# Performance work log

Measured on AMD Instinct MI355X. Metric: run time of the kernel, lower is better.

Reference implementation:

```python
import jax, jax.numpy as jnp
import numpy as np
import math

DIM, SCALES, ORIENTS, K = 32, 3, 8, 15
SIGMA, GAMMA = 5.0, 0.5
B, H, W = 4, 128, 128

def _make_gabor_filters():
    # matches EnhancedBlockGabor._create_complex_filters
    coords = np.arange(-(K // 2), K // 2 + 1, dtype=np.float32)
    y, x = np.meshgrid(coords, coords, indexing='ij')  # torch.meshgrid default 'ij'
    filts = []
    for s in range(SCALES):
        fu = 1.0 / 2 ** s
        for o in range(ORIENTS):
            theta = o * math.pi / ORIENTS
            xt = x * math.cos(theta) + y * math.sin(theta)
            yt = -x * math.sin(theta) + y * math.cos(theta)
            env = np.exp(-(xt ** 2 + GAMMA ** 2 * yt ** 2) / (2 * SIGMA ** 2))
            amp = fu ** 2 / (math.pi * GAMMA ** 2)
            real = amp * env * np.cos(2 * math.pi * fu * xt)
            imag = amp * env * np.sin(2 * math.pi * fu * xt)
            filts.append(np.stack([real, imag]))
    return jnp.asarray(np.stack(filts), dtype=jnp.float32)  # (S*O, 2, K, K)

def setup_inputs() -> dict:
    key = jax.random.key(0)
    k1, k2, k3 = jax.random.split(key, 3)
    x = jax.random.normal(k1, (B, DIM, H, W), dtype=jnp.float32)
    filters = _make_gabor_filters()
    cin = DIM * SCALES * ORIENTS
    w1 = jax.random.normal(k2, (DIM, cin), dtype=jnp.float32) / np.sqrt(cin)
    b1 = jax.random.normal(k3, (DIM,), dtype=jnp.float32) * 0.01
    return {"x": x, "filters": filters, "w1": w1, "b1": b1}

def reference(x, filters, w1, b1):
    Bb, C, Hh, Ww = x.shape
    SO = filters.shape[0]
    pad = K // 2
    # depthwise multi-scale Gabor conv: every channel vs every (scale,orient,re/im) filter
    xr = x.reshape(Bb * C, 1, Hh, Ww)
    kern = filters.reshape(SO * 2, 1, K, K)
    feat = jax.lax.conv_general_dilated(
        xr, kern, window_strides=(1, 1), padding=[(pad, pad), (pad, pad)],
        dimension_numbers=('NCHW', 'OIHW', 'NCHW'))  # (B*C, SO*2, H, W)
    feat = feat.reshape(Bb, C, SO, 2, Hh, Ww)
    mag = jnp.sqrt(feat[:, :, :, 0] ** 2 + feat[:, :, :, 1] ** 2)  # (B,C,SO,H,W)
    mag = jnp.swapaxes(mag, -1, -2)  # original permutes H<->W before reshape
    mag = mag.reshape(Bb, C * SO, Hh, Ww)
    y = jnp.einsum('oc,bchw->bohw', w1, mag) + b1[None, :, None, None]
    mean = y.mean(axis=(2, 3), keepdims=True)
    var = y.var(axis=(2, 3), keepdims=True)
    return (y - mean) / jnp.sqrt(var + 1e-5)  # InstanceNorm2d (affine=False)
```

## Files before the change

### kernel.cpp

```cpp
#include <hip/hip_runtime.h>


typedef __attribute__((ext_vector_type(8))) short bfx8;
typedef __attribute__((ext_vector_type(4))) float fx4;
typedef __attribute__((ext_vector_type(4))) unsigned ux4;

#define NREP   2
#define RPITCH 144
#define RROWS  144
#define IMG_SH (RROWS * RPITCH)
#define REP_SH (128 * IMG_SH)
#define XREP_SH (NREP * REP_SH)

#define A_OFF    ((size_t)XREP_SH * 2)
#define W1B_OFF  (A_OFF + (size_t)48 * 256 * 2)
#define YP_OFF   (W1B_OFF + (size_t)32 * 32 * 32 * 2)
#define ST_OFF   (YP_OFF + (size_t)128 * 16384 * 4)

#define WROW_DW  40
#define WREP_DW  656
#define WBUF_DW  (2 * WREP_DW)
#define WWAVE_DW (2 * WBUF_DW)

__device__ __forceinline__ unsigned short f2bf(float f) {
    unsigned u = __float_as_uint(f);
    u = (u + 0x7FFFu + ((u >> 16) & 1u)) >> 16;
    return (unsigned short)u;
}

__device__ __forceinline__ float fsqrt(float x) {
    float r;
    asm("v_sqrt_f32 %0, %1" : "=v"(r) : "v"(x));
    return r;
}

__global__ void prep(const float* __restrict__ x, const float* __restrict__ filt,
                     const float* __restrict__ w1, unsigned* __restrict__ xrep,
                     unsigned short* __restrict__ A, unsigned short* __restrict__ w1b,
                     float* __restrict__ stats)
{
    const int bid = blockIdx.x;
    if (bid < 2048) {
        const int phi = bid & 1, img = (bid >> 1) & 127, rg = bid >> 8;
        const unsigned obase = (unsigned)phi * (REP_SH / 2) + img * (IMG_SH / 2)
                             + rg * 18 * 72;
        for (int j = threadIdx.x; j < 18 * 72; j += 256) {
            int jr = j / 72;
            int pd = j - jr * 72;
            int r  = rg * 18 + jr;
            int c0 = 2 * pd + phi;
            float v0 = 0.f, v1 = 0.f;
            int rr = r - 7;
            if (rr >= 0 && rr < 128) {
                const float* row = x + ((size_t)img * 128 + rr) * 128;
                int cc0 = c0 - 7;
                if (cc0 >= 0 && cc0 < 128) v0 = row[cc0];
                int cc1 = c0 - 6;
                if (cc1 >= 0 && cc1 < 128) v1 = row[cc1];
            }
            xrep[obase + j] = (unsigned)f2bf(v0) | ((unsigned)f2bf(v1) << 16);
        }
    } else {
        int t = (bid - 2048) * 256 + threadIdx.x;
        if (t < 48 * 256) {
            int f = t >> 8, k = t & 255;
            int ky = k >> 4, kx = k & 15;
            float v = 0.f;
            if (ky < 15 && kx < 15) v = filt[(f * 15 + ky) * 15 + kx];
            A[t] = f2bf(v);
        } else if (t < 48 * 256 + 32 * 32 * 32) {
            int j = t - 48 * 256;
            int c = j >> 10, o = (j >> 5) & 31, so = j & 31;
            float v = (so < 24) ? w1[o * 768 + c * 24 + so] : 0.f;
            w1b[j] = f2bf(v);
        } else if (t < 48 * 256 + 32 * 32 * 32 + 256) {
            stats[t - (48 * 256 + 32 * 32 * 32)] = 0.f;
        }
    }
}

__global__ void __attribute__((amdgpu_waves_per_eu(2, 2)))
__launch_bounds__(256)
conv_mix(const unsigned short* __restrict__ xrep,
         const unsigned short* __restrict__ Aw,
         const unsigned short* __restrict__ w1b,
         float* __restrict__ ypart, float* __restrict__ stats)
{
    __shared__ unsigned stagew[4 * WWAVE_DW];
    __shared__ unsigned mag_lds[4][32][20];
    __shared__ float stat_lds[4][4][16];

    const int tid  = threadIdx.x;
    const int lane = tid & 63;
    const int wave = tid >> 6;
    const int n    = lane & 15;
    const int q    = lane >> 4;

    const int bid = blockIdx.x;
    const int b   = (bid >> 1) & 3;
    const int h   = (bid & 1) * 64 + (bid >> 3);

    if (lane < 32) {
        ux4 z4 = {0u, 0u, 0u, 0u};
        *(ux4*)&mag_lds[wave][lane][12] = z4;
    }

    ux4 afr[3][8];
#pragma unroll
    for (int mt = 0; mt < 3; ++mt)
#pragma unroll
        for (int s = 0; s < 8; ++s)
            afr[mt][s] = *(const ux4*)(Aw + ((mt * 16 + n) * 256 + s * 32 + q * 8));
#pragma unroll
    for (int mt = 0; mt < 3; ++mt)
#pragma unroll
        for (int s = 0; s < 8; ++s)
            asm volatile("" : "+v"(afr[mt][s]));

    const int px0 = wave * 32;
    const int p   = n & 1;
    const int fbase = wave * WWAVE_DW + p * WREP_DW + (q >> 1) * WROW_DW
                    + ((n - p) >> 1) + (q & 1) * 4;

    int g_off[3], l_off[3];
#pragma unroll
    for (int i = 0; i < 3; ++i) {
        int slot = i * 64 + lane;
        int rep  = slot >= 96;
        int rem  = slot - 96 * rep;
        int row  = rem / 6;
        int sl   = rem - row * 6;
        g_off[i] = rep * REP_SH + (h + row) * RPITCH + px0 + sl * 8;
        l_off[i] = wave * WWAVE_DW + rep * WREP_DW + row * WROW_DW + sl * 4;
    }
    const int imgbase0 = (b * 32) * IMG_SH;

    const fx4 zero4 = {0.f, 0.f, 0.f, 0.f};
    fx4 yacc[2][2];
#pragma unroll
    for (int mt = 0; mt < 2; ++mt)
#pragma unroll
        for (int t = 0; t < 2; ++t) yacc[mt][t] = zero4;

    {
        const unsigned short* g = xrep + imgbase0;
#pragma unroll
        for (int i = 0; i < 3; ++i)
            *(ux4*)&stagew[l_off[i]] = *(const ux4*)(g + g_off[i]);
    }

    for (int c = 0; c < 32; ++c) {
        ux4 nv[3];
        if (c < 31) {
            const unsigned short* g = xrep + imgbase0 + (c + 1) * IMG_SH;
#pragma unroll
            for (int i = 0; i < 3; ++i)
                nv[i] = *(const ux4*)(g + g_off[i]);
        }

        bfx8 wf[2];
#pragma unroll
        for (int mt = 0; mt < 2; ++mt)
            wf[mt] = *(const bfx8*)(w1b + ((c * 32 + mt * 16 + n) * 32 + q * 8));

        const int fb = fbase + (c & 1) * WBUF_DW;
        ux4 braw[2][8];
#pragma unroll
        for (int s = 0; s < 8; ++s)
#pragma unroll
            for (int t = 0; t < 2; ++t) {
                const int ix = fb + s * (2 * WROW_DW) + t * 8;
                ux4 v = {stagew[ix], stagew[ix + 1], stagew[ix + 2], stagew[ix + 3]};
                braw[t][s] = v;
            }
#pragma unroll
        for (int s = 0; s < 8; ++s)
#pragma unroll
            for (int t = 0; t < 2; ++t)
                asm volatile("" : "+v"(braw[t][s]));

        fx4 cacc[3][2];
#pragma unroll
        for (int mt = 0; mt < 3; ++mt)
#pragma unroll
            for (int t = 0; t < 2; ++t) cacc[mt][t] = zero4;

#pragma unroll
        for (int s = 0; s < 8; ++s)
#pragma unroll
            for (int t = 0; t < 2; ++t) {
                bfx8 bf = __builtin_bit_cast(bfx8, braw[t][s]);
#pragma unroll
                for (int mt = 0; mt < 3; ++mt)
                    cacc[mt][t] = __builtin_amdgcn_mfma_f32_16x16x32_bf16(
                        __builtin_bit_cast(bfx8, afr[mt][s]), bf, cacc[mt][t], 0, 0, 0);
            }

#pragma unroll
        for (int t = 0; t < 2; ++t)
#pragma unroll
            for (int mt = 0; mt < 3; ++mt) {
                float m0 = fsqrt(cacc[mt][t][0] * cacc[mt][t][0] +
                                 cacc[mt][t][1] * cacc[mt][t][1]);
                float m1 = fsqrt(cacc[mt][t][2] * cacc[mt][t][2] +
                                 cacc[mt][t][3] * cacc[mt][t][3]);
                unsigned u0 = __float_as_uint(m0), u1 = __float_as_uint(m1);
                unsigned pk = ((u0 + 0x8000u) >> 16) | ((u1 + 0x8000u) & 0xFFFF0000u);
                mag_lds[wave][t * 16 + n][4 * mt + q] = pk;
            }

#pragma unroll
        for (int t = 0; t < 2; ++t) {
            ux4 raw = *(const ux4*)&mag_lds[wave][t * 16 + n][q * 4];
            bfx8 mb = __builtin_bit_cast(bfx8, raw);
#pragma unroll
            for (int mt = 0; mt < 2; ++mt)
                yacc[mt][t] = __builtin_amdgcn_mfma_f32_16x16x32_bf16(
                    wf[mt], mb, yacc[mt][t], 0, 0, 0);
        }

        if (c < 31) {
            const int wb = ((c + 1) & 1) * WBUF_DW;
#pragma unroll
            for (int i = 0; i < 3; ++i)
                *(ux4*)&stagew[wb + l_off[i]] = nv[i];
        }
    }

    float* yp = ypart + (size_t)(b * 32) * 16384 + h * 128;
#pragma unroll
    for (int mt = 0; mt < 2; ++mt)
#pragma unroll
        for (int t = 0; t < 2; ++t) {
            const int w0 = px0 + t * 16 + n;
#pragma unroll
            for (int r = 0; r < 4; ++r)
                yp[(size_t)(mt * 16 + 4 * q + r) * 16384 + w0] = yacc[mt][t][r];
        }

    float sv[8], qv[8];
#pragma unroll
    for (int mt = 0; mt < 2; ++mt)
#pragma unroll
        for (int r = 0; r < 4; ++r) {
            float v0 = yacc[mt][0][r], v1 = yacc[mt][1][r];
            sv[mt * 4 + r] = v0 + v1;
            qv[mt * 4 + r] = v0 * v0 + v1 * v1;
        }
#pragma unroll
    for (int m = 1; m <= 8; m <<= 1)
#pragma unroll
        for (int i = 0; i < 8; ++i) {
            sv[i] += __shfl_xor(sv[i], m);
            qv[i] += __shfl_xor(qv[i], m);
        }
    if (n == 0) {
#pragma unroll
        for (int i = 0; i < 8; ++i) {
            stat_lds[wave][q][i]     = sv[i];
            stat_lds[wave][q][i + 8] = qv[i];
        }
    }
    __syncthreads();
    if (tid < 64) {
        int qq = tid >> 4, i = tid & 15;
        float acc = stat_lds[0][qq][i] + stat_lds[1][qq][i] +
                    stat_lds[2][qq][i] + stat_lds[3][qq][i];
        int kind = i >> 3, mt = (i >> 2) & 1, r = i & 3;
        int o = mt * 16 + 4 * qq + r;
        atomicAdd(&stats[(b * 32 + o) * 2 + kind], acc);
    }
}

__global__ void inorm2(const float* __restrict__ ypart, const float* __restrict__ stats,
                       float* __restrict__ out)
{
    const int bid = blockIdx.x;
    const int bo = bid >> 4, tile = bid & 15;
    const int h0 = (tile >> 2) * 32, w0 = (tile & 3) * 32;
    const float mean = stats[bo * 2] * (1.f / 16384.f);
    float var = stats[bo * 2 + 1] * (1.f / 16384.f) - mean * mean;
    const float rstd = rsqrtf(fmaxf(var, 0.f) + 1e-5f);

    const float* y0 = ypart + (size_t)bo * 16384;
    __shared__ float tilebuf[32][33];
    const int r = threadIdx.x >> 3, c4 = (threadIdx.x & 7) * 4;

    const size_t base = (size_t)(h0 + r) * 128 + w0 + c4;
    fx4 a = *(const fx4*)(y0 + base);
#pragma unroll
    for (int j = 0; j < 4; ++j)
        tilebuf[r][c4 + j] = (a[j] - mean) * rstd;
    __syncthreads();
    float* ob = out + (size_t)bo * 16384 + (size_t)(w0 + r) * 128 + h0 + c4;
    fx4 o4;
#pragma unroll
    for (int j = 0; j < 4; ++j) o4[j] = tilebuf[c4 + j][r];
    *(fx4*)ob = o4;
}

extern "C" void kernel_launch(void* const* d_in, const int* in_sizes, int n_in,
                              void* d_out, int out_size, void* d_ws, size_t ws_size,
                              hipStream_t stream)
{
    const float* x    = (const float*)d_in[0];
    const float* filt = (const float*)d_in[1];
    const float* w1   = (const float*)d_in[2];
    float* out = (float*)d_out;
    char* ws = (char*)d_ws;

    unsigned*       xrep  = (unsigned*)ws;
    unsigned short* Aw    = (unsigned short*)(ws + A_OFF);
    unsigned short* w1b   = (unsigned short*)(ws + W1B_OFF);
    float*          yp    = (float*)(ws + YP_OFF);
    float*          stats = (float*)(ws + ST_OFF);

    prep<<<2048 + 178, 256, 0, stream>>>(x, filt, w1, xrep, Aw, w1b, stats);
    conv_mix<<<512, 256, 0, stream>>>((const unsigned short*)xrep, Aw, w1b, yp, stats);
    inorm2<<<2048, 256, 0, stream>>>(yp, stats, out);
}
```

Baseline: 127.2 us.

## Software-pipeline mixing MFMA one channel behind and stream B-fragment LDS loads

Double-buffers the per-wave magnitude LDS tile so that the 1x1 mixing MFMAs for channel c-1 run inside the Gabor conv MFMA loop of channel c. This hides the LDS write-then-read dependency. The B-fragment loads become a two-deep rolling prefetch per k-step instead of loading all 8 steps up front, which lowers VGPR pressure. The cost is extra LDS for the second magnitude buffer, a carried weight register pair, and an epilogue for the last channel. Less upfront loading could expose LDS latency if the scheduler does not overlap it.

Measured after the change: 126.2 us. Within noise of the previous version (-0.8%).

```diff
diff --git a/kernel.cpp b/kernel.cpp
--- a/kernel.cpp
+++ b/kernel.cpp
@@ -87,7 +87,7 @@
          float* __restrict__ ypart, float* __restrict__ stats)
 {
     __shared__ unsigned stagew[4 * WWAVE_DW];
-    __shared__ unsigned mag_lds[4][32][20];
+    __shared__ unsigned mag_lds[2][4][32][20];
     __shared__ float stat_lds[4][4][16];
 
     const int tid  = threadIdx.x;
@@ -102,7 +102,8 @@
 
     if (lane < 32) {
         ux4 z4 = {0u, 0u, 0u, 0u};
-        *(ux4*)&mag_lds[wave][lane][12] = z4;
+        *(ux4*)&mag_lds[0][wave][lane][12] = z4;
+        *(ux4*)&mag_lds[1][wave][lane][12] = z4;
     }
 
     ux4 afr[3][8];
@@ -149,6 +150,8 @@
             *(ux4*)&stagew[l_off[i]] = *(const ux4*)(g + g_off[i]);
     }
 
+    bfx8 wfp[2];
+
     for (int c = 0; c < 32; ++c) {
         ux4 nv[3];
         if (c < 31) {
@@ -158,43 +161,64 @@
                 nv[i] = *(const ux4*)(g + g_off[i]);
         }
 
-        bfx8 wf[2];
+        ux4 magp[2];
+        if (c > 0) {
+            const int pbuf = (c & 1) ^ 1;
+#pragma unroll
+            for (int t = 0; t < 2; ++t)
+                magp[t] = *(const ux4*)&mag_lds[pbuf][wave][t * 16 + n][q * 4];
+        }
+
+        bfx8 wfc[2];
 #pragma unroll
         for (int mt = 0; mt < 2; ++mt)
-            wf[mt] = *(const bfx8*)(w1b + ((c * 32 + mt * 16 + n) * 32 + q * 8));
+            wfc[mt] = *(const bfx8*)(w1b + ((c * 32 + mt * 16 + n) * 32 + q * 8));
 
         const int fb = fbase + (c & 1) * WBUF_DW;
-        ux4 braw[2][8];
-#pragma unroll
-        for (int s = 0; s < 8; ++s)
+        ux4 braw[2][2];
+#pragma unroll
+        for (int t = 0; t < 2; ++t) {
+            const int ix = fb + t * 8;
+            ux4 v = {stagew[ix], stagew[ix + 1], stagew[ix + 2], stagew[ix + 3]};
+            braw[0][t] = v;
+        }
+
+        fx4 cacc[3][2];
+#pragma unroll
+        for (int mt = 0; mt < 3; ++mt)
+#pragma unroll
+            for (int t = 0; t < 2; ++t) cacc[mt][t] = zero4;
+
+#pragma unroll
+        for (int s = 0; s < 8; ++s) {
+            if (s < 7) {
+#pragma unroll
+                for (int t = 0; t < 2; ++t) {
+                    const int ix = fb + (s + 1) * (2 * WROW_DW) + t * 8;
+                    ux4 v = {stagew[ix], stagew[ix + 1],
+                             stagew[ix + 2], stagew[ix + 3]};
+                    braw[(s + 1) & 1][t] = v;
+                }
+            }
 #pragma unroll
             for (int t = 0; t < 2; ++t) {
-                const int ix = fb + s * (2 * WROW_DW) + t * 8;
-                ux4 v = {stagew[ix], stagew[ix + 1], stagew[ix + 2], stagew[ix + 3]};
-                braw[t][s] = v;
-            }
-#pragma unroll
-        for (int s = 0; s < 8; ++s)
-#pragma unroll
-            for (int t = 0; t < 2; ++t)
-                asm volatile("" : "+v"(braw[t][s]));
-
-        fx4 cacc[3][2];
-#pragma unroll
-        for (int mt = 0; mt < 3; ++mt)
-#pragma unroll
-            for (int t = 0; t < 2; ++t) cacc[mt][t] = zero4;
-
-#pragma unroll
-        for (int s = 0; s < 8; ++s)
-#pragma unroll
-            for (int t = 0; t < 2; ++t) {
-                bfx8 bf = __builtin_bit_cast(bfx8, braw[t][s]);
+                bfx8 bf = __builtin_bit_cast(bfx8, braw[s & 1][t]);
 #pragma unroll
                 for (int mt = 0; mt < 3; ++mt)
                     cacc[mt][t] = __builtin_amdgcn_mfma_f32_16x16x32_bf16(
                         __builtin_bit_cast(bfx8, afr[mt][s]), bf, cacc[mt][t], 0, 0, 0);
             }
+            if (s == 1 && c > 0) {
+#pragma unroll
+                for (int t = 0; t < 2; ++t) {
+                    bfx8 mb = __builtin_bit_cast(bfx8, magp[t]);
+#pragma unroll
+                    for (int mt = 0; mt < 2; ++mt)
+                        yacc[mt][t] = __builtin_amdgcn_mfma_f32_16x16x32_bf16(
+                            wfp[mt], mb, yacc[mt][t], 0, 0, 0);
+                }
+            }
+        }
 
 #pragma unroll
         for (int t = 0; t < 2; ++t)
@@ -206,18 +230,8 @@
                                  cacc[mt][t][3] * cacc[mt][t][3]);
                 unsigned u0 = __float_as_uint(m0), u1 = __float_as_uint(m1);
                 unsigned pk = ((u0 + 0x8000u) >> 16) | ((u1 + 0x8000u) & 0xFFFF0000u);
-                mag_lds[wave][t * 16 + n][4 * mt + q] = pk;
-            }
-
-#pragma unroll
-        for (int t = 0; t < 2; ++t) {
-            ux4 raw = *(const ux4*)&mag_lds[wave][t * 16 + n][q * 4];
-            bfx8 mb = __builtin_bit_cast(bfx8, raw);
-#pragma unroll
-            for (int mt = 0; mt < 2; ++mt)
-                yacc[mt][t] = __builtin_amdgcn_mfma_f32_16x16x32_bf16(
-                    wf[mt], mb, yacc[mt][t], 0, 0, 0);
-        }
+                mag_lds[c & 1][wave][t * 16 + n][4 * mt + q] = pk;
+            }
 
         if (c < 31) {
             const int wb = ((c + 1) & 1) * WBUF_DW;
@@ -225,6 +239,18 @@
             for (int i = 0; i < 3; ++i)
                 *(ux4*)&stagew[wb + l_off[i]] = nv[i];
         }
+#pragma unroll
+        for (int mt = 0; mt < 2; ++mt) wfp[mt] = wfc[mt];
+    }
+
+#pragma unroll
+    for (int t = 0; t < 2; ++t) {
+        ux4 raw = *(const ux4*)&mag_lds[1][wave][t * 16 + n][q * 4];
+        bfx8 mb = __builtin_bit_cast(bfx8, raw);
+#pragma unroll
+        for (int mt = 0; mt < 2; ++mt)
+            yacc[mt][t] = __builtin_amdgcn_mfma_f32_16x16x32_bf16(
+                wfp[mt], mb, yacc[mt][t], 0, 0, 0);
     }
 
     float* yp = ypart + (size_t)(b * 32) * 16384 + h * 128;
```
